# Kernel optimization log

Measured on AMD Instinct MI355X. Metric: run time of the kernel, lower is better.

Reference implementation:

```python
import jax, jax.numpy as jnp
import numpy as np

VOCAB = 50257
EMBED_DIM = 128
TOP_N = 8
B, LQ, LC = 4, 128, 65536


def setup_inputs() -> dict:
    key = jax.random.key(0)
    k1, k2, k3, k4 = jax.random.split(key, 4)
    query_tokens = jax.random.randint(k1, (B, LQ), 0, VOCAB, dtype=jnp.int32)
    context_tokens = jax.random.randint(k2, (LC,), 0, VOCAB, dtype=jnp.int32)
    emb_table = jax.random.normal(k3, (VOCAB, EMBED_DIM), dtype=jnp.float32) * 0.02
    W_score = jax.random.normal(k4, (EMBED_DIM, EMBED_DIM), dtype=jnp.float32) / np.sqrt(EMBED_DIM)
    b_score = jnp.zeros((EMBED_DIM,), dtype=jnp.float32)
    return {
        "query_tokens": query_tokens,
        "context_tokens": context_tokens,
        "emb_table": emb_table,
        "W_score": W_score,
        "b_score": b_score,
    }


def reference(query_tokens, context_tokens, emb_table, W_score, b_score):
    # --- TokenEmbedder: embedding lookups ---
    q = emb_table[query_tokens]        # [B, Lq, D]
    c = emb_table[context_tokens]      # [Lc, D]

    # --- ExploratoryMechanism: euclidean distance + top_n nearest ---
    # ||q - c||^2 = ||q||^2 + ||c||^2 - 2 q.c
    sq = (jnp.sum(q * q, axis=-1)[..., None]
          + jnp.sum(c * c, axis=-1)[None, None, :]
          - 2.0 * jnp.einsum('bqd,cd->bqc', q, c))      # [B, Lq, Lc]
    dist = jnp.sqrt(jnp.maximum(sq, 0.0) + 1e-12)
    neg_top, top_n_indices = jax.lax.top_k(-dist, TOP_N)  # smallest distances
    top_n_distances = -neg_top                             # [B, Lq, n]

    # --- gather top-n context embeddings ---
    top_n_embeddings = c[top_n_indices]                    # [B, Lq, n, D]

    # --- RAGScorer: projected dot-product score penalized by distance ---
    qp = q @ W_score + b_score                             # [B, Lq, D]
    logits = (jnp.einsum('bqd,bqnd->bqn', qp, top_n_embeddings)
              / np.sqrt(EMBED_DIM)) - top_n_distances      # [B, Lq, n]
    rag_scores = jax.nn.softmax(logits, axis=-1)           # [B, Lq, n]

    # --- QueryReconstructor: score-driven reweighting of query positions ---
    importance = jnp.max(rag_scores, axis=-1)              # [B, Lq]
    weights = jax.nn.softmax(importance, axis=-1)          # [B, Lq]
    lq = query_tokens.shape[1]
    reconstructed_query = query_tokens.astype(jnp.float32) * weights * lq
    return reconstructed_query
```

## Files before the change

kernel.cpp:

```cpp
#include <hip/hip_runtime.h>
#include <math.h>

#define D      128
#define NQ     512
#define LCTX   65536
#define TOPN   8
#define NCAND  16
#define QT     64
#define CCHUNK 512
#define CSTEP  128
#define NCH    (LCTX / CCHUNK)
#define PERCHUNK 16
#define NCANDTOT (NCH * PERCHUNK)
#define NQT    (NQ / QT)
#define NROWS  (LCTX + NQ)
#define FINF   3.0e38f

typedef __attribute__((ext_vector_type(8))) __bf16 bf16x8;
typedef __attribute__((ext_vector_type(4))) float f32x4;

static __device__ __forceinline__ unsigned pack2(float a, float b) {
  const unsigned ua = (__float_as_uint(a) + 0x8000u) >> 16;
  const unsigned ub = (__float_as_uint(b) + 0x8000u) & 0xffff0000u;
  return ua | ub;
}

__global__ __launch_bounds__(256) void pack_kernel(const int* __restrict__ ctok,
                                                   const int* __restrict__ qtok,
                                                   const float* __restrict__ emb,
                                                   unsigned short* __restrict__ cemb,
                                                   float* __restrict__ cn2) {
  const int g = threadIdx.x >> 5, l = threadIdx.x & 31;
  const int row = blockIdx.x * 8 + g;
  const int tok = (row < LCTX) ? ctok[row] : qtok[row - LCTX];
  const float4 v = *(const float4*)(emb + (size_t)tok * D + 4 * l);
  float p = v.x * v.x + v.y * v.y + v.z * v.z + v.w * v.w;
#pragma unroll
  for (int off = 16; off; off >>= 1) p += __shfl_xor(p, off, 32);
  if (l == 0 && row < LCTX) cn2[row] = p;
  const int c = l >> 1, h = l & 1;
  const int pch = c ^ (row & 7);
  uint2 pk = make_uint2(pack2(v.x, v.y), pack2(v.z, v.w));
  *(uint2*)(&cemb[(size_t)row * D + pch * 8 + h * 4]) = pk;
}

__global__ __launch_bounds__(256) void qprep_kernel(const int* __restrict__ qtok,
                                                    const float* __restrict__ emb,
                                                    const float* __restrict__ W,
                                                    const float* __restrict__ bvec,
                                                    float* __restrict__ qp) {
  __shared__ float sW[D * D];
  __shared__ float sq[8][D];
  const int tid = threadIdx.x;
  const int qb = blockIdx.x * 8;
#pragma unroll
  for (int j = 0; j < 16; ++j) {
    const int i4 = j * 256 + tid;
    *(float4*)(&sW[i4 * 4]) = *(const float4*)(W + i4 * 4);
  }
  {
    const int r = tid >> 5, l = tid & 31;
    const int tok = qtok[qb + r];
    *(float4*)(&sq[r][4 * l]) = *(const float4*)(emb + (size_t)tok * D + 4 * l);
  }
  __syncthreads();
  const int d = tid & 127, qs = tid >> 7;
  const float bv = bvec[d];
  float acc[4] = {bv, bv, bv, bv};
  for (int k = 0; k < D; ++k) {
    const float wv = sW[k * D + d];
#pragma unroll
    for (int i = 0; i < 4; ++i) acc[i] = fmaf(sq[2 * i + qs][k], wv, acc[i]);
  }
#pragma unroll
  for (int i = 0; i < 4; ++i) qp[(size_t)(qb + 2 * i + qs) * D + d] = acc[i];
}

__global__ __launch_bounds__(256, 4) void dist_topk_kernel(
    const unsigned short* __restrict__ cemb, const float* __restrict__ cn2,
    float2* __restrict__ partials) {
  __shared__ __align__(16) unsigned short sCt[CSTEP * D];
  __shared__ __align__(16) float scn2[CCHUNK];

  const int tid = threadIdx.x;
  const int wid = tid >> 6, lane = tid & 63;
  const int n = lane & 15, qq = lane >> 4;
  const int chunk = blockIdx.x, qtile = blockIdx.y;
  const int qbase = qtile * QT, cbase0 = chunk * CCHUNK;

  scn2[tid] = cn2[cbase0 + tid];
  scn2[tid + 256] = cn2[cbase0 + tid + 256];

  {
    const unsigned short* qrowbase = cemb + (size_t)(LCTX + qbase) * D;
#pragma unroll
    for (int j = 0; j < 4; ++j) {
      const int r0 = wid * 16 + j * 4;
      const unsigned short* gp = qrowbase + r0 * D + lane * 8;
      __builtin_amdgcn_global_load_lds(
          (const __attribute__((address_space(1))) unsigned int*)gp,
          (__attribute__((address_space(3))) unsigned int*)&sCt[r0 * D], 16, 0, 0);
    }
  }
  __syncthreads();

  bf16x8 bq[4];
  {
    const int rq = wid * 16 + n;
#pragma unroll
    for (int kk = 0; kk < 4; ++kk)
      bq[kk] = *(const bf16x8*)(&sCt[rq * D + 8 * ((4 * kk + qq) ^ (rq & 7))]);
  }

  float bs[4] = {FINF, FINF, FINF, FINF};
  int bi[4] = {0, 0, 0, 0};

  for (int st = 0; st < CCHUNK / CSTEP; ++st) {
    const int cb = cbase0 + st * CSTEP;
    __syncthreads();
    {
      const unsigned short* crowbase = cemb + (size_t)cb * D;
#pragma unroll
      for (int j = 0; j < 8; ++j) {
        const int r0 = wid * 32 + j * 4;
        const unsigned short* gp = crowbase + r0 * D + lane * 8;
        __builtin_amdgcn_global_load_lds(
            (const __attribute__((address_space(1))) unsigned int*)gp,
            (__attribute__((address_space(3))) unsigned int*)&sCt[r0 * D], 16, 0, 0);
      }
    }
    __syncthreads();

#pragma unroll
    for (int tt = 0; tt < 8; ++tt) {
      f32x4 acc = {0.f, 0.f, 0.f, 0.f};
      const int m = 16 * tt + n;
#pragma unroll
      for (int kk = 0; kk < 4; ++kk) {
        const bf16x8 af = *(const bf16x8*)(&sCt[m * D + 8 * ((4 * kk + qq) ^ (n & 7))]);
        acc = __builtin_amdgcn_mfma_f32_16x16x32_bf16(af, bq[kk], acc, 0, 0, 0);
      }
      const f32x4 cv = *(const f32x4*)(&scn2[st * CSTEP + 16 * tt + 4 * qq]);
      const int ibase = cb + 16 * tt + 4 * qq;
#pragma unroll
      for (int r = 0; r < 4; ++r) {
        const float v = fmaf(-2.f, acc[r], cv[r]);
        const int iv = ibase + r;
        const bool c0 = v < bs[0], c1 = v < bs[1], c2 = v < bs[2], c3 = v < bs[3];
        const float nb0 = fminf(bs[0], v);
        const float nb1 = __builtin_amdgcn_fmed3f(v, bs[0], bs[1]);
        const float nb2 = __builtin_amdgcn_fmed3f(v, bs[1], bs[2]);
        const float nb3 = __builtin_amdgcn_fmed3f(v, bs[2], bs[3]);
        const int ni0 = c0 ? iv : bi[0];
        const int ni1 = c1 ? (c0 ? bi[0] : iv) : bi[1];
        const int ni2 = c2 ? (c1 ? bi[1] : iv) : bi[2];
        const int ni3 = c3 ? (c2 ? bi[2] : iv) : bi[3];
        bs[0] = nb0; bs[1] = nb1; bs[2] = nb2; bs[3] = nb3;
        bi[0] = ni0; bi[1] = ni1; bi[2] = ni2; bi[3] = ni3;
      }
    }
  }

  const int q = qbase + wid * 16 + n;
  float2* dst = partials + (size_t)q * NCANDTOT + chunk * PERCHUNK + qq * 4;
#pragma unroll
  for (int t = 0; t < 4; ++t)
    dst[t] = make_float2(bs[t], __int_as_float(bi[t]));
}

__global__ __launch_bounds__(256) void select_kernel(
    const float2* __restrict__ partials, const int* __restrict__ qtok,
    const int* __restrict__ ctok, const float* __restrict__ emb,
    const float* __restrict__ qp, float* __restrict__ importance) {
  __shared__ float2 swt[64];
  __shared__ double sd2[NCAND], sdp[NCAND];
  __shared__ int sid[NCAND];
  const int tid = threadIdx.x;
  const int w = tid >> 6, lane = tid & 63;
  const int q = blockIdx.x;

  float v[8]; int vi[8];
  const float2* pq = partials + (size_t)q * NCANDTOT;
#pragma unroll
  for (int j = 0; j < 8; ++j) {
    const float2 cd = pq[256 * j + tid];
    v[j] = cd.x; vi[j] = __float_as_int(cd.y);
  }
  unsigned consumed = 0;
#pragma unroll
  for (int t = 0; t < NCAND; ++t) {
    float lmin = FINF; int li = 0x7fffffff; int ls = 0;
#pragma unroll
    for (int j = 0; j < 8; ++j) {
      const bool take = !((consumed >> j) & 1u) && (v[j] < lmin);
      lmin = take ? v[j] : lmin;
      li = take ? vi[j] : li;
      ls = take ? j : ls;
    }
    float m = lmin; int pidx = li; int pwho = (lane << 3) | ls;
#pragma unroll
    for (int off = 32; off; off >>= 1) {
      const float om = __shfl_xor(m, off, 64);
      const int oi = __shfl_xor(pidx, off, 64);
      const int ow = __shfl_xor(pwho, off, 64);
      const bool better = (om < m) || (om == m && oi < pidx);
      m = better ? om : m; pidx = better ? oi : pidx; pwho = better ? ow : pwho;
    }
    if ((pwho >> 3) == lane) consumed |= 1u << (pwho & 7);
    if (lane == t) swt[w * 16 + t] = make_float2(m, __int_as_float(pidx));
  }
  __syncthreads();

  if (w == 0) {
    const float2 cd = swt[lane];
    const float mv = cd.x; const int mi = __float_as_int(cd.y);
    bool cons = false;
#pragma unroll
    for (int t = 0; t < NCAND; ++t) {
      float m = cons ? FINF : mv;
      int pidx = cons ? 0x7fffffff : mi;
      int pwho = lane;
#pragma unroll
      for (int off = 32; off; off >>= 1) {
        const float om = __shfl_xor(m, off, 64);
        const int oi = __shfl_xor(pidx, off, 64);
        const int ow = __shfl_xor(pwho, off, 64);
        const bool better = (om < m) || (om == m && oi < pidx);
        m = better ? om : m; pidx = better ? oi : pidx; pwho = better ? ow : pwho;
      }
      if (pwho == lane) cons = true;
      if (lane == t) sid[t] = pidx;
    }
  }
  __syncthreads();

  const int c = tid >> 4, sub = tid & 15;
  const int idx = sid[c];
  const int tc = ctok[idx];
  const int tq = qtok[q];
  const float* crow = emb + (size_t)tc * D + sub * 8;
  const float* qrow = emb + (size_t)tq * D + sub * 8;
  const float* prow = qp + (size_t)q * D + sub * 8;
  double dd = 0.0, pp = 0.0;
#pragma unroll
  for (int kk = 0; kk < 2; ++kk) {
    const float4 cv = *(const float4*)(crow + 4 * kk);
    const float4 qv = *(const float4*)(qrow + 4 * kk);
    const float4 pv = *(const float4*)(prow + 4 * kk);
    const double dx = (double)qv.x - (double)cv.x, dy = (double)qv.y - (double)cv.y;
    const double dz = (double)qv.z - (double)cv.z, dw = (double)qv.w - (double)cv.w;
    dd += dx * dx + dy * dy + dz * dz + dw * dw;
    pp += (double)pv.x * (double)cv.x + (double)pv.y * (double)cv.y +
          (double)pv.z * (double)cv.z + (double)pv.w * (double)cv.w;
  }
#pragma unroll
  for (int off = 1; off <= 8; off <<= 1) {
    dd += __shfl_xor(dd, off, 64);
    pp += __shfl_xor(pp, off, 64);
  }
  if (sub == 0) { sd2[c] = dd; sdp[c] = pp; }
  __syncthreads();

  if (tid == 0) {
    bool used[NCAND];
#pragma unroll
    for (int n2 = 0; n2 < NCAND; ++n2) used[n2] = false;
    double lg[TOPN];
    for (int t = 0; t < TOPN; ++t) {
      int best = -1;
      for (int n2 = 0; n2 < NCAND; ++n2) {
        if (used[n2]) continue;
        if (best < 0 || sd2[n2] < sd2[best] ||
            (sd2[n2] == sd2[best] && sid[n2] < sid[best])) best = n2;
      }
      used[best] = true;
      lg[t] = sdp[best] * 0.08838834764831843 - sqrt(sd2[best] + 1e-12);
    }
    double m = lg[0];
#pragma unroll
    for (int t = 1; t < TOPN; ++t) m = fmax(m, lg[t]);
    double sum = 0.0;
#pragma unroll
    for (int t = 0; t < TOPN; ++t) sum += exp(lg[t] - m);
    importance[q] = (float)(1.0 / sum);
  }
}

__global__ __launch_bounds__(128) void out_kernel(const float* __restrict__ importance,
                                                  const int* __restrict__ qtok,
                                                  float* __restrict__ out) {
  const int b = blockIdx.x, i = threadIdx.x;
  __shared__ double sred[2];
  const double v = (double)importance[b * 128 + i];
  double m = v;
#pragma unroll
  for (int off = 32; off; off >>= 1) m = fmax(m, __shfl_xor(m, off, 64));
  if ((i & 63) == 0) sred[i >> 6] = m;
  __syncthreads();
  const double M = fmax(sred[0], sred[1]);
  const double e = exp(v - M);
  double s = e;
#pragma unroll
  for (int off = 32; off; off >>= 1) s += __shfl_xor(s, off, 64);
  __syncthreads();
  if ((i & 63) == 0) sred[i >> 6] = s;
  __syncthreads();
  const double S = sred[0] + sred[1];
  out[b * 128 + i] = (float)((double)qtok[b * 128 + i] * (e / S) * 128.0);
}

extern "C" void kernel_launch(void* const* d_in, const int* in_sizes, int n_in,
                              void* d_out, int out_size, void* d_ws, size_t ws_size,
                              hipStream_t stream) {
  const int* qtok = (const int*)d_in[0];
  const int* ctok = (const int*)d_in[1];
  const float* emb = (const float*)d_in[2];
  const float* W = (const float*)d_in[3];
  const float* bvec = (const float*)d_in[4];
  float* out = (float*)d_out;

  char* ws = (char*)d_ws;
  float* cn2 = (float*)ws;
  float* qp = cn2 + LCTX;
  float* imp = qp + (size_t)NQ * D;
  unsigned short* cemb = (unsigned short*)(imp + NQ);
  float2* partials = (float2*)(cemb + (size_t)NROWS * D);

  pack_kernel<<<NROWS / 8, 256, 0, stream>>>(ctok, qtok, emb, cemb, cn2);
  qprep_kernel<<<NQ / 8, 256, 0, stream>>>(qtok, emb, W, bvec, qp);
  dist_topk_kernel<<<dim3(NCH, NQT), 256, 0, stream>>>(cemb, cn2, partials);
  select_kernel<<<NQ, 256, 0, stream>>>(partials, qtok, ctok, emb, qp, imp);
  out_kernel<<<4, 128, 0, stream>>>(imp, qtok, out);
}
```

Baseline: 150.8 us.

## Merge pack and qprep kernels, double query tile with 512-thread blocks

Fuses the context packing and query projection kernels into one launch, with the projection streaming W through shared memory in 32-row chunks to cut LDS use. The distance/top-k kernel now handles 128 queries per block with 512 threads, so each context tile loaded into LDS is reused across twice as many queries and the per-thread staging load count halves. The select kernel reads partials as float4 pairs instead of float2. The aim is fewer launches and less context reload traffic, at the cost of larger blocks that may lower occupancy.

After: 153.1 us. Within noise of the previous version (+1.5%).

```diff
diff --git a/kernel.cpp b/kernel.cpp
--- a/kernel.cpp
+++ b/kernel.cpp
@@ -6,7 +6,7 @@
 #define LCTX   65536
 #define TOPN   8
 #define NCAND  16
-#define QT     64
+#define QT     128
 #define CCHUNK 512
 #define CSTEP  128
 #define NCH    (LCTX / CCHUNK)
@@ -14,6 +14,8 @@
 #define NCANDTOT (NCH * PERCHUNK)
 #define NQT    (NQ / QT)
 #define NROWS  (LCTX + NQ)
+#define PACKB  (NROWS / 8)
+#define QPREPB (NQ / 8)
 #define FINF   3.0e38f
 
 typedef __attribute__((ext_vector_type(8))) __bf16 bf16x8;
@@ -25,58 +27,64 @@
   return ua | ub;
 }
 
-__global__ __launch_bounds__(256) void pack_kernel(const int* __restrict__ ctok,
+__global__ __launch_bounds__(256) void prep_kernel(const int* __restrict__ ctok,
                                                    const int* __restrict__ qtok,
                                                    const float* __restrict__ emb,
+                                                   const float* __restrict__ W,
+                                                   const float* __restrict__ bvec,
                                                    unsigned short* __restrict__ cemb,
-                                                   float* __restrict__ cn2) {
-  const int g = threadIdx.x >> 5, l = threadIdx.x & 31;
-  const int row = blockIdx.x * 8 + g;
-  const int tok = (row < LCTX) ? ctok[row] : qtok[row - LCTX];
-  const float4 v = *(const float4*)(emb + (size_t)tok * D + 4 * l);
-  float p = v.x * v.x + v.y * v.y + v.z * v.z + v.w * v.w;
-#pragma unroll
-  for (int off = 16; off; off >>= 1) p += __shfl_xor(p, off, 32);
-  if (l == 0 && row < LCTX) cn2[row] = p;
-  const int c = l >> 1, h = l & 1;
-  const int pch = c ^ (row & 7);
-  uint2 pk = make_uint2(pack2(v.x, v.y), pack2(v.z, v.w));
-  *(uint2*)(&cemb[(size_t)row * D + pch * 8 + h * 4]) = pk;
-}
-
-__global__ __launch_bounds__(256) void qprep_kernel(const int* __restrict__ qtok,
-                                                    const float* __restrict__ emb,
-                                                    const float* __restrict__ W,
-                                                    const float* __restrict__ bvec,
-                                                    float* __restrict__ qp) {
-  __shared__ float sW[D * D];
+                                                   float* __restrict__ cn2,
+                                                   float* __restrict__ qp) {
+  __shared__ float sW[32 * D];
   __shared__ float sq[8][D];
   const int tid = threadIdx.x;
-  const int qb = blockIdx.x * 8;
-#pragma unroll
-  for (int j = 0; j < 16; ++j) {
-    const int i4 = j * 256 + tid;
-    *(float4*)(&sW[i4 * 4]) = *(const float4*)(W + i4 * 4);
-  }
+
+  if (blockIdx.x < PACKB) {
+    const int g = tid >> 5, l = tid & 31;
+    const int row = blockIdx.x * 8 + g;
+    const int tok = (row < LCTX) ? ctok[row] : qtok[row - LCTX];
+    const float4 v = *(const float4*)(emb + (size_t)tok * D + 4 * l);
+    float p = v.x * v.x + v.y * v.y + v.z * v.z + v.w * v.w;
+#pragma unroll
+    for (int off = 16; off; off >>= 1) p += __shfl_xor(p, off, 32);
+    if (l == 0 && row < LCTX) cn2[row] = p;
+    const int c = l >> 1, h = l & 1;
+    const int pch = c ^ (row & 7);
+    uint2 pk = make_uint2(pack2(v.x, v.y), pack2(v.z, v.w));
+    *(uint2*)(&cemb[(size_t)row * D + pch * 8 + h * 4]) = pk;
+    return;
+  }
+
+  const int qb = (blockIdx.x - PACKB) * 8;
   {
     const int r = tid >> 5, l = tid & 31;
     const int tok = qtok[qb + r];
     *(float4*)(&sq[r][4 * l]) = *(const float4*)(emb + (size_t)tok * D + 4 * l);
   }
-  __syncthreads();
   const int d = tid & 127, qs = tid >> 7;
   const float bv = bvec[d];
   float acc[4] = {bv, bv, bv, bv};
-  for (int k = 0; k < D; ++k) {
-    const float wv = sW[k * D + d];
-#pragma unroll
-    for (int i = 0; i < 4; ++i) acc[i] = fmaf(sq[2 * i + qs][k], wv, acc[i]);
+  for (int ch = 0; ch < 4; ++ch) {
+    __syncthreads();
+#pragma unroll
+    for (int j = 0; j < 4; ++j) {
+      const int i4 = j * 256 + tid;
+      *(float4*)(&sW[i4 * 4]) = *(const float4*)(W + (size_t)ch * 32 * D + i4 * 4);
+    }
+    __syncthreads();
+#pragma unroll
+    for (int kk = 0; kk < 32; ++kk) {
+      const float wv = sW[kk * D + d];
+      const int k = ch * 32 + kk;
+#pragma unroll
+      for (int i = 0; i < 4; ++i) acc[i] = fmaf(sq[2 * i + qs][k], wv, acc[i]);
+    }
   }
 #pragma unroll
   for (int i = 0; i < 4; ++i) qp[(size_t)(qb + 2 * i + qs) * D + d] = acc[i];
 }
 
-__global__ __launch_bounds__(256, 4) void dist_topk_kernel(
+__global__ __launch_bounds__(512, 4) void dist_topk_kernel(
     const unsigned short* __restrict__ cemb, const float* __restrict__ cn2,
     float2* __restrict__ partials) {
   __shared__ __align__(16) unsigned short sCt[CSTEP * D];
@@ -89,7 +97,6 @@
   const int qbase = qtile * QT, cbase0 = chunk * CCHUNK;
 
   scn2[tid] = cn2[cbase0 + tid];
-  scn2[tid + 256] = cn2[cbase0 + tid + 256];
 
   {
     const unsigned short* qrowbase = cemb + (size_t)(LCTX + qbase) * D;
@@ -121,8 +128,8 @@
     {
       const unsigned short* crowbase = cemb + (size_t)cb * D;
 #pragma unroll
-      for (int j = 0; j < 8; ++j) {
-        const int r0 = wid * 32 + j * 4;
+      for (int j = 0; j < 4; ++j) {
+        const int r0 = wid * 16 + j * 4;
         const unsigned short* gp = crowbase + r0 * D + lane * 8;
         __builtin_amdgcn_global_load_lds(
             (const __attribute__((address_space(1))) unsigned int*)gp,
@@ -180,11 +187,12 @@
   const int q = blockIdx.x;
 
   float v[8]; int vi[8];
-  const float2* pq = partials + (size_t)q * NCANDTOT;
-#pragma unroll
-  for (int j = 0; j < 8; ++j) {
-    const float2 cd = pq[256 * j + tid];
-    v[j] = cd.x; vi[j] = __float_as_int(cd.y);
+  const float4* pq4 = (const float4*)(partials + (size_t)q * NCANDTOT);
+#pragma unroll
+  for (int j = 0; j < 4; ++j) {
+    const float4 cd = pq4[256 * j + tid];
+    v[2 * j] = cd.x;     vi[2 * j] = __float_as_int(cd.y);
+    v[2 * j + 1] = cd.z; vi[2 * j + 1] = __float_as_int(cd.w);
   }
   unsigned consumed = 0;
 #pragma unroll
@@ -326,9 +334,9 @@
   unsigned short* cemb = (unsigned short*)(imp + NQ);
   float2* partials = (float2*)(cemb + (size_t)NROWS * D);
 
-  pack_kernel<<<NROWS / 8, 256, 0, stream>>>(ctok, qtok, emb, cemb, cn2);
-  qprep_kernel<<<NQ / 8, 256, 0, stream>>>(qtok, emb, W, bvec, qp);
-  dist_topk_kernel<<<dim3(NCH, NQT), 256, 0, stream>>>(cemb, cn2, partials);
+  prep_kernel<<<PACKB + QPREPB, 256, 0, stream>>>(ctok, qtok, emb, W, bvec,
+                                                  cemb, cn2, qp);
+  dist_topk_kernel<<<dim3(NCH, NQT), 512, 0, stream>>>(cemb, cn2, partials);
   select_kernel<<<NQ, 256, 0, stream>>>(partials, qtok, ctok, emb, qp, imp);
   out_kernel<<<4, 128, 0, stream>>>(imp, qtok, out);
 }
```
